# Performance work log

Hardware: AMD Instinct MI355X
Metric: run time of the kernel (lower is better)

The kernel has to match this reference:

```python
import jax, jax.numpy as jnp
import numpy as np

B, S, D, H, DF = 8, 1024, 1024, 16, 4096
DK = D // H
EPS = 1e-5


def setup_inputs() -> dict:
    key = jax.random.key(0)
    ks = jax.random.split(key, 16)
    w = lambda k, shape: (jax.random.normal(k, shape, jnp.float32) * 0.02)
    inp = {
        "x": jax.random.normal(ks[0], (B, S, D), jnp.float32),
        "mask": jnp.ones((B, 1, 1, S), jnp.int32),
        # attention projections (torch Linear: y = x @ W.T + b)
        "Wq": w(ks[1], (D, D)), "bq": jnp.zeros((D,), jnp.float32),
        "Wk": w(ks[2], (D, D)), "bk": jnp.zeros((D,), jnp.float32),
        "Wv": w(ks[3], (D, D)), "bv": jnp.zeros((D,), jnp.float32),
        "Wo": w(ks[4], (D, D)), "bo": jnp.zeros((D,), jnp.float32),
        "ln_attn_g": jnp.ones((D,), jnp.float32), "ln_attn_b": jnp.zeros((D,), jnp.float32),
        # feed-forward
        "W1": w(ks[5], (DF, D)), "b1": jnp.zeros((DF,), jnp.float32),
        "W2": w(ks[6], (D, DF)), "b2": jnp.zeros((D,), jnp.float32),
        "ln_ff_g": jnp.ones((D,), jnp.float32), "ln_ff_b": jnp.zeros((D,), jnp.float32),
        # BatchNorm1d(d_ff) inside FFN (eval mode: running stats)
        "bnff_g": jnp.ones((DF,), jnp.float32), "bnff_b": jnp.zeros((DF,), jnp.float32),
        "bnff_m": jnp.zeros((DF,), jnp.float32), "bnff_v": jnp.ones((DF,), jnp.float32),
        # BatchNorm1d(d_model) after each sublayer (eval mode)
        "bn1_g": jnp.ones((D,), jnp.float32), "bn1_b": jnp.zeros((D,), jnp.float32),
        "bn1_m": jnp.zeros((D,), jnp.float32), "bn1_v": jnp.ones((D,), jnp.float32),
        "bn2_g": jnp.ones((D,), jnp.float32), "bn2_b": jnp.zeros((D,), jnp.float32),
        "bn2_m": jnp.zeros((D,), jnp.float32), "bn2_v": jnp.ones((D,), jnp.float32),
    }
    return inp


def _layernorm(x, g, b):
    mu = jnp.mean(x, axis=-1, keepdims=True)
    var = jnp.mean(jnp.square(x - mu), axis=-1, keepdims=True)
    return (x - mu) * jax.lax.rsqrt(var + EPS) * g + b


def _batchnorm_eval(x, g, b, m, v):
    # x: [B,S,C]; BatchNorm1d over channel C (the transpose->bn->transpose in torch
    # is equivalent to per-channel affine normalization on the last dim in eval mode)
    return (x - m) * jax.lax.rsqrt(v + EPS) * g + b


def reference(x, mask, Wq, bq, Wk, bk, Wv, bv, Wo, bo, ln_attn_g, ln_attn_b,
              W1, b1, W2, b2, ln_ff_g, ln_ff_b,
              bnff_g, bnff_b, bnff_m, bnff_v,
              bn1_g, bn1_b, bn1_m, bn1_v,
              bn2_g, bn2_b, bn2_m, bn2_v):
    # ---- Multi-head self-attention (pre-LN on query/key/value input) ----
    xq = _layernorm(x, ln_attn_g, ln_attn_b)
    q = (xq @ Wq.T + bq).reshape(B, S, H, DK)
    k = (x @ Wk.T + bk).reshape(B, S, H, DK)   # note: original applies LN only to `query`;
    v = (x @ Wv.T + bv).reshape(B, S, H, DK)   # key/value are passed raw (same x here)
    scores = jnp.einsum("bqhd,bkhd->bhqk", q, k) / np.sqrt(DK).astype(np.float32)
    scores = jnp.where(mask == 0, jnp.float32(-1e9), scores)
    attn = jax.nn.softmax(scores, axis=-1)                      # [B,H,S,S]
    context = jnp.einsum("bhqk,bkhd->bqhd", attn, v).reshape(B, S, D)
    attn_out = context @ Wo.T + bo
    x = x + attn_out                                            # residual (eval: no dropout)
    x = _batchnorm_eval(x, bn1_g, bn1_b, bn1_m, bn1_v)
    # ---- Position-wise FFN ----
    xn = _layernorm(x, ln_ff_g, ln_ff_b)
    h = jax.nn.gelu(xn @ W1.T + b1, approximate=False)          # [B,S,DF]
    h = _batchnorm_eval(h, bnff_g, bnff_b, bnff_m, bnff_v)
    ff = h @ W2.T + b2
    x = x + ff
    x = _batchnorm_eval(x, bn2_g, bn2_b, bn2_m, bn2_v)
    return x, attn
```

## Files before the change

kernel.cpp:

```cpp
#include <hip/hip_runtime.h>
#include <hip/hip_bf16.h>
#include <math.h>

typedef __hip_bfloat16 bf16;
typedef __attribute__((ext_vector_type(8))) short short8;
typedef __attribute__((ext_vector_type(4))) short short4v;
typedef __attribute__((ext_vector_type(4))) float f32x4;

#define DEV static __device__ __forceinline__

DEV short f2bf(float f) {
    bf16 h = __float2bfloat16(f);
    return __builtin_bit_cast(short, h);
}

DEV void glds16(const void* g, void* l) {
    __builtin_amdgcn_global_load_lds((const __attribute__((address_space(1))) void*)g,
                                     (__attribute__((address_space(3))) void*)l, 16, 0, 0);
}

__global__ __launch_bounds__(256) void cast_all(const float* __restrict__ Wq,
                                                const float* __restrict__ Wk,
                                                const float* __restrict__ Wv,
                                                const float* __restrict__ Wo,
                                                const float* __restrict__ W1,
                                                const float* __restrict__ W2,
                                                bf16* __restrict__ wqkv, bf16* __restrict__ wo,
                                                bf16* __restrict__ w1, bf16* __restrict__ w2) {
    int i = blockIdx.x * 256 + threadIdx.x;
    const float* src;
    bf16* dst;
    int si, di;
    if (i < 786432) {
        src = (i < 262144) ? Wq : (i < 524288) ? Wk : Wv;
        si = (i < 262144) ? i : (i < 524288) ? i - 262144 : i - 524288;
        dst = wqkv; di = i;
    } else if (i < 1048576) {
        src = Wo; si = i - 786432; dst = wo; di = si;
    } else if (i < 2097152) {
        src = W1; si = i - 1048576; dst = w1; di = si;
    } else {
        src = W2; si = i - 2097152; dst = w2; di = si;
    }
    f32x4 v = ((const f32x4*)src)[si];
    short4v o;
    #pragma unroll
    for (int j = 0; j < 4; j++) o[j] = f2bf(v[j]);
    ((short4v*)dst)[di] = o;
}

__global__ __launch_bounds__(256) void affine_all(
    const float* __restrict__ g1, const float* __restrict__ bb1, const float* __restrict__ m1, const float* __restrict__ v1,
    const float* __restrict__ g2, const float* __restrict__ bb2, const float* __restrict__ m2, const float* __restrict__ v2,
    const float* __restrict__ gf, const float* __restrict__ bbf, const float* __restrict__ mf, const float* __restrict__ vf,
    float* __restrict__ s1, float* __restrict__ t1, float* __restrict__ s2, float* __restrict__ t2,
    float* __restrict__ sf, float* __restrict__ tf) {
    int i = blockIdx.x * 256 + threadIdx.x;
    const float *g, *b, *m, *v; float *s, *t; int j;
    if (i < 1024)      { g = g1; b = bb1; m = m1; v = v1; s = s1; t = t1; j = i; }
    else if (i < 2048) { g = g2; b = bb2; m = m2; v = v2; s = s2; t = t2; j = i - 1024; }
    else               { g = gf; b = bbf; m = mf; v = vf; s = sf; t = tf; j = i - 2048; }
    float sc = g[j] * rsqrtf(v[j] + 1e-5f);
    s[j] = sc;
    t[j] = b[j] - m[j] * sc;
}

__global__ __launch_bounds__(256) void ln_kernel(const float* __restrict__ x,
                                                 const float* __restrict__ g,
                                                 const float* __restrict__ b,
                                                 bf16* __restrict__ lnout,
                                                 bf16* __restrict__ rawout) {
    const int row = blockIdx.x, t = threadIdx.x;
    const float* xr = x + (size_t)row * 1024;
    f32x4 v = ((const f32x4*)xr)[t];
    float s = v[0] + v[1] + v[2] + v[3];
    float sq = v[0]*v[0] + v[1]*v[1] + v[2]*v[2] + v[3]*v[3];
    #pragma unroll
    for (int off = 1; off < 64; off <<= 1) {
        s  += __shfl_xor(s, off);
        sq += __shfl_xor(sq, off);
    }
    __shared__ float ls[4], lq[4];
    if ((t & 63) == 0) { ls[t >> 6] = s; lq[t >> 6] = sq; }
    __syncthreads();
    s = ls[0] + ls[1] + ls[2] + ls[3];
    sq = lq[0] + lq[1] + lq[2] + lq[3];
    float mu = s * (1.0f / 1024.0f);
    float rs = rsqrtf(sq * (1.0f / 1024.0f) - mu * mu + 1e-5f);
    f32x4 gg = ((const f32x4*)g)[t];
    f32x4 bb = ((const f32x4*)b)[t];
    short4v o;
    #pragma unroll
    for (int j = 0; j < 4; j++) o[j] = f2bf((v[j] - mu) * rs * gg[j] + bb[j]);
    ((short4v*)(lnout + (size_t)row * 1024))[t] = o;
    if (rawout) {
        short4v r;
        #pragma unroll
        for (int j = 0; j < 4; j++) r[j] = f2bf(v[j]);
        ((short4v*)(rawout + (size_t)row * 1024))[t] = r;
    }
}

enum { M_RESBN = 0, M_GELU = 1, M_QKV = 2 };

template <int BN, int MODE>
__global__ __launch_bounds__(512, 2) void gemm8(
    const bf16* __restrict__ A0, const bf16* __restrict__ A1, const bf16* __restrict__ Bw,
    const float* __restrict__ b0, const float* __restrict__ b1, const float* __restrict__ b2,
    void* __restrict__ o0, void* __restrict__ o1, void* __restrict__ o2,
    const float* __restrict__ res, const float* __restrict__ sa, const float* __restrict__ ta,
    int N, int K) {
    constexpr int NB = BN / 64;
    constexpr int SB = BN * 128;
    constexpr int CW = BN / 4;
    constexpr int NF = CW / 16;
    __shared__ char smem[65536 + 2 * SB];

    const int tid = threadIdx.x, lane = tid & 63, wid = tid >> 6;
    const int gx = gridDim.x;
    const int n_wg = gx * gridDim.y;
    int lin = blockIdx.y * gx + blockIdx.x;
    lin = (lin & 7) * (n_wg >> 3) + (lin >> 3);
    const int bn = (lin % gx) * BN, bm = (lin / gx) << 8;

    const int wr = wid >> 2, wc = wid & 3;
    const int arow = lane & 15, hi = lane >> 4;
    const int xr = arow & 7;
    const int ck0 = (hi ^ xr) << 3;
    const int ck1 = ((4 + hi) ^ xr) << 3;
    const int rowA = wr * 128 + arow;
    const int rowB = wc * CW + arow;

    const bf16* Asel;
    if constexpr (MODE == M_QKV) Asel = (bn < 1024) ? A0 : A1;
    else                         Asel = A0;

    const int rS = tid >> 3;
    const int cXor = ((tid & 7) ^ (rS & 7)) << 3;
    const bf16* gA = Asel + (size_t)(bm + rS) * K + cXor;
    const bf16* gB = Bw   + (size_t)(bn + rS) * K + cXor;

    f32x4 acc[8][NF] = {};

    auto stA = [&](int t, int i) {
        glds16(gA + (size_t)i * 64 * K + t * 64,
               smem + ((t & 1) << 15) + i * 8192 + (wid << 10));
    };
    auto stB = [&](int t, int i) {
        glds16(gB + (size_t)i * 64 * K + t * 64,
               smem + 65536 + (t & 1) * SB + i * 8192 + (wid << 10));
    };

    const int NT = K >> 6;
    #pragma unroll
    for (int i = 0; i < NB; i++) stB(0, i);
    stA(0, 0); stA(0, 2); stA(0, 1); stA(0, 3);

#define PHASE(Q)                                                                              \
    do {                                                                                      \
        const short8 a00 = *(const short8*)(Ap + (rowA + (2*(Q)) * 16) * 64 + ck0);           \
        const short8 a01 = *(const short8*)(Ap + (rowA + (2*(Q)) * 16) * 64 + ck1);           \
        const short8 a10 = *(const short8*)(Ap + (rowA + (2*(Q)+1) * 16) * 64 + ck0);         \
        const short8 a11 = *(const short8*)(Ap + (rowA + (2*(Q)+1) * 16) * 64 + ck1);         \
        __builtin_amdgcn_s_setprio(1);                                                        \
        _Pragma("unroll")                                                                     \
        for (int n = 0; n < NF; n++) {                                                        \
            acc[2*(Q)][n]   = __builtin_amdgcn_mfma_f32_16x16x32_bf16(a00, bva[n], acc[2*(Q)][n], 0, 0, 0);   \
            acc[2*(Q)][n]   = __builtin_amdgcn_mfma_f32_16x16x32_bf16(a01, bvb[n], acc[2*(Q)][n], 0, 0, 0);   \
            acc[2*(Q)+1][n] = __builtin_amdgcn_mfma_f32_16x16x32_bf16(a10, bva[n], acc[2*(Q)+1][n], 0, 0, 0); \
            acc[2*(Q)+1][n] = __builtin_amdgcn_mfma_f32_16x16x32_bf16(a11, bvb[n], acc[2*(Q)+1][n], 0, 0, 0); \
        }                                                                                     \
        __builtin_amdgcn_s_setprio(0);                                                        \
    } while (0)

    for (int t = 0; t < NT; ++t) {
        const int p = t & 1;
        const bf16* Ap = (const bf16*)(smem + (p << 15));
        const bf16* Bp = (const bf16*)(smem + 65536 + p * SB);
        asm volatile("s_waitcnt vmcnt(2)" ::: "memory");
        __builtin_amdgcn_s_barrier();
        if (t + 1 < NT) {
            stB(t + 1, 0);
            if constexpr (NB == 4) stB(t + 1, 1);
        }
        short8 bva[NF], bvb[NF];
        #pragma unroll
        for (int n = 0; n < NF; n++) {
            bva[n] = *(const short8*)(Bp + (rowB + n * 16) * 64 + ck0);
            bvb[n] = *(const short8*)(Bp + (rowB + n * 16) * 64 + ck1);
        }
        PHASE(0);
        __builtin_amdgcn_s_barrier();
        if (t + 1 < NT) {
            if constexpr (NB == 4) { stB(t + 1, 2); stB(t + 1, 3); }
            else                   { stB(t + 1, 1); }
        }
        PHASE(1);
        if (t == NT - 1) asm volatile("s_waitcnt vmcnt(0)" ::: "memory");
        else if constexpr (NB == 4) asm volatile("s_waitcnt vmcnt(4)" ::: "memory");
        else                        asm volatile("s_waitcnt vmcnt(2)" ::: "memory");
        __builtin_amdgcn_s_barrier();
        if (t + 1 < NT) { stA(t + 1, 0); stA(t + 1, 2); }
        PHASE(2);
        __builtin_amdgcn_s_barrier();
        if (t + 1 < NT) { stA(t + 1, 1); stA(t + 1, 3); }
        PHASE(3);
    }
#undef PHASE

    #pragma unroll
    for (int mf = 0; mf < 8; mf++) {
        #pragma unroll
        for (int nf = 0; nf < NF; nf++) {
            const int col = bn + wc * CW + nf * 16 + arow;
            #pragma unroll
            for (int j = 0; j < 4; j++) {
                const int row = bm + wr * 128 + mf * 16 + hi * 4 + j;
                if constexpr (MODE == M_RESBN) {
                    float v = acc[mf][nf][j] + b0[col];
                    size_t idx = (size_t)row * N + col;
                    ((float*)o0)[idx] = (res[idx] + v) * sa[col] + ta[col];
                } else if constexpr (MODE == M_GELU) {
                    float v = acc[mf][nf][j] + b0[col];
                    float ge = 0.5f * v * (1.0f + erff(v * 0.70710678118f));
                    ((bf16*)o0)[(size_t)row * N + col] = __float2bfloat16(ge * sa[col] + ta[col]);
                } else {
                    const int reg = col >> 10, c = col & 1023;
                    const float bb = (reg == 0) ? b0[c] : (reg == 1) ? b1[c] : b2[c];
                    float v = acc[mf][nf][j] + bb;
                    if (reg == 0)
                        ((bf16*)o0)[(size_t)row * 1024 + c] = __float2bfloat16(v * 0.125f);
                    else if (reg == 1)
                        ((bf16*)o1)[(size_t)row * 1024 + c] = __float2bfloat16(v);
                    else
                        ((bf16*)o2)[((size_t)(row >> 10) << 20) + ((size_t)c << 10) + (row & 1023)] =
                            __float2bfloat16(v);
                }
            }
        }
    }
}

__global__ __launch_bounds__(512, 4) void fattn_kernel(const bf16* __restrict__ q,
                                                       const bf16* __restrict__ k,
                                                       const bf16* __restrict__ vT,
                                                       const int* __restrict__ mask,
                                                       float* __restrict__ attn,
                                                       bf16* __restrict__ ctx) {
    const int bh = blockIdx.y, b = bh >> 4, h = bh & 15;
    const int q0 = blockIdx.x << 5;
    const int tid = threadIdx.x, lane = tid & 63, wid = tid >> 6;
    const int kb = wid << 7;
    const int arow = lane & 15, hi = lane >> 4, koff = hi << 3;
    const int rbase = hi << 2;

    __shared__ char smem[67584];
    bf16* Plds = (bf16*)smem;
    float* redm = (float*)(smem + 65536);
    float* reds = (float*)(smem + 66560);

    short8 qf[2], qf2[2];
    #pragma unroll
    for (int m = 0; m < 2; m++) {
        const bf16* qp = q + ((size_t)((b << 10) + q0 + (m << 4) + arow) << 10) + (h << 6);
        qf[m]  = *(const short8*)(qp + koff);
        qf2[m] = *(const short8*)(qp + 32 + koff);
    }

    f32x4 acc[2][8];
    #pragma unroll
    for (int m = 0; m < 2; m++)
        #pragma unroll
        for (int n = 0; n < 8; n++) acc[m][n] = (f32x4){0.f, 0.f, 0.f, 0.f};

    const bf16* kpBase = k + ((size_t)((b << 10) + kb + arow) << 10) + (h << 6);
    short8 kf  = *(const short8*)(kpBase + koff);
    short8 kf2 = *(const short8*)(kpBase + 32 + koff);
    #pragma unroll
    for (int n = 0; n < 8; n++) {
        short8 kfn, kf2n;
        if (n < 7) {
            const bf16* kp = kpBase + ((size_t)(n + 1) << 14);
            kfn  = *(const short8*)(kp + koff);
            kf2n = *(const short8*)(kp + 32 + koff);
        }
        acc[0][n] = __builtin_amdgcn_mfma_f32_16x16x32_bf16(qf[0],  kf,  acc[0][n], 0, 0, 0);
        acc[0][n] = __builtin_amdgcn_mfma_f32_16x16x32_bf16(qf2[0], kf2, acc[0][n], 0, 0, 0);
        acc[1][n] = __builtin_amdgcn_mfma_f32_16x16x32_bf16(qf[1],  kf,  acc[1][n], 0, 0, 0);
        acc[1][n] = __builtin_amdgcn_mfma_f32_16x16x32_bf16(qf2[1], kf2, acc[1][n], 0, 0, 0);
        kf = kfn; kf2 = kf2n;
    }

    float rmax[2][4];
    #pragma unroll
    for (int m = 0; m < 2; m++)
        #pragma unroll
        for (int j = 0; j < 4; j++) rmax[m][j] = -3.0e38f;

    #pragma unroll
    for (int n = 0; n < 8; n++) {
        const float madd = mask[(b << 10) + kb + (n << 4) + arow] ? 0.0f : -1e9f;
        #pragma unroll
        for (int m = 0; m < 2; m++)
            #pragma unroll
            for (int j = 0; j < 4; j++) {
                acc[m][n][j] += madd;
                rmax[m][j] = fmaxf(rmax[m][j], acc[m][n][j]);
            }
    }
    #pragma unroll
    for (int off = 1; off < 16; off <<= 1)
        #pragma unroll
        for (int m = 0; m < 2; m++)
            #pragma unroll
            for (int j = 0; j < 4; j++) rmax[m][j] = fmaxf(rmax[m][j], __shfl_xor(rmax[m][j], off));

    float rsum[2][4] = {};
    #pragma unroll
    for (int n = 0; n < 8; n++)
        #pragma unroll
        for (int m = 0; m < 2; m++)
            #pragma unroll
            for (int j = 0; j < 4; j++) {
                float p = __expf(acc[m][n][j] - rmax[m][j]);
                acc[m][n][j] = p;
                rsum[m][j] += p;
            }
    #pragma unroll
    for (int off = 1; off < 16; off <<= 1)
        #pragma unroll
        for (int m = 0; m < 2; m++)
            #pragma unroll
            for (int j = 0; j < 4; j++) rsum[m][j] += __shfl_xor(rsum[m][j], off);

    if (arow == 0) {
        #pragma unroll
        for (int m = 0; m < 2; m++)
            #pragma unroll
            for (int j = 0; j < 4; j++) {
                const int qr = (m << 4) + rbase + j;
                redm[(qr << 3) + wid] = rmax[m][j];
                reds[(qr << 3) + wid] = rsum[m][j];
            }
    }
    __syncthreads();

    float fscale[2][4];
    #pragma unroll
    for (int m = 0; m < 2; m++)
        #pragma unroll
        for (int j = 0; j < 4; j++) {
            const int qr = (m << 4) + rbase + j;
            const float* mm = redm + (qr << 3);
            const float* ss = reds + (qr << 3);
            f32x4 m0 = *(const f32x4*)mm, m1 = *(const f32x4*)(mm + 4);
            f32x4 s0 = *(const f32x4*)ss, s1 = *(const f32x4*)(ss + 4);
            float gm = fmaxf(fmaxf(fmaxf(m0[0], m0[1]), fmaxf(m0[2], m0[3])),
                             fmaxf(fmaxf(m1[0], m1[1]), fmaxf(m1[2], m1[3])));
            float S = s0[0] * __expf(m0[0] - gm) + s0[1] * __expf(m0[1] - gm) +
                      s0[2] * __expf(m0[2] - gm) + s0[3] * __expf(m0[3] - gm) +
                      s1[0] * __expf(m1[0] - gm) + s1[1] * __expf(m1[1] - gm) +
                      s1[2] * __expf(m1[2] - gm) + s1[3] * __expf(m1[3] - gm);
            fscale[m][j] = __expf(rmax[m][j] - gm) / S;
        }

    const size_t obase = (((size_t)bh << 10) + q0) << 10;
    #pragma unroll
    for (int m = 0; m < 2; m++)
        #pragma unroll
        for (int j = 0; j < 4; j++) {
            const int qr = (m << 4) + rbase + j;
            float* orow = attn + obase + ((size_t)qr << 10) + kb;
            char* prow = (char*)Plds + (qr << 11);
            const int rx = (qr & 7) << 4;
            const float iv = fscale[m][j];
            #pragma unroll
            for (int n = 0; n < 8; n++) {
                float p = acc[m][n][j] * iv;
                orow[(n << 4) + arow] = p;
                *(bf16*)(prow + ((((kb + (n << 4) + arow)) << 1) ^ rx)) = __float2bfloat16(p);
            }
        }

    asm volatile("s_waitcnt lgkmcnt(0)" ::: "memory");
    __builtin_amdgcn_s_barrier();
    __builtin_amdgcn_sched_barrier(0);

    const int qh = wid >> 2, dh = wid & 3;
    const char* pbase = (char*)Plds + (((qh << 4) + arow) << 11);
    const int prx = (arow & 7) << 4;
    const bf16* vrow = vT + ((size_t)((b << 10) + (h << 6) + (dh << 4) + arow) << 10);
    f32x4 acc2 = (f32x4){0.f, 0.f, 0.f, 0.f};
    #pragma unroll 8
    for (int kt = 0; kt < 32; kt++) {
        short8 af  = *(const short8*)(pbase + (((kt << 6) + (hi << 4)) ^ prx));
        short8 bf2 = *(const short8*)(vrow + (kt << 5) + koff);
        acc2 = __builtin_amdgcn_mfma_f32_16x16x32_bf16(af, bf2, acc2, 0, 0, 0);
    }

    #pragma unroll
    for (int j = 0; j < 4; j++) {
        const int row = q0 + (qh << 4) + rbase + j;
        ctx[((size_t)((b << 10) + row) << 10) + (h << 6) + (dh << 4) + arow] =
            __float2bfloat16(acc2[j]);
    }
}

extern "C" void kernel_launch(void* const* d_in, const int* in_sizes, int n_in,
                              void* d_out, int out_size, void* d_ws, size_t ws_size,
                              hipStream_t stream) {
    (void)in_sizes; (void)n_in; (void)out_size; (void)ws_size;
    const float* x   = (const float*)d_in[0];
    const int*   mask= (const int*)d_in[1];
    const float* Wq  = (const float*)d_in[2];  const float* bq  = (const float*)d_in[3];
    const float* Wk  = (const float*)d_in[4];  const float* bk  = (const float*)d_in[5];
    const float* Wv  = (const float*)d_in[6];  const float* bv  = (const float*)d_in[7];
    const float* Wo  = (const float*)d_in[8];  const float* bo  = (const float*)d_in[9];
    const float* lag = (const float*)d_in[10]; const float* lab = (const float*)d_in[11];
    const float* W1  = (const float*)d_in[12]; const float* b1  = (const float*)d_in[13];
    const float* W2  = (const float*)d_in[14]; const float* b2  = (const float*)d_in[15];
    const float* lfg = (const float*)d_in[16]; const float* lfb = (const float*)d_in[17];
    const float* bffg= (const float*)d_in[18]; const float* bffb= (const float*)d_in[19];
    const float* bffm= (const float*)d_in[20]; const float* bffv= (const float*)d_in[21];
    const float* b1g = (const float*)d_in[22]; const float* b1b = (const float*)d_in[23];
    const float* b1m = (const float*)d_in[24]; const float* b1v = (const float*)d_in[25];
    const float* b2g = (const float*)d_in[26]; const float* b2b = (const float*)d_in[27];
    const float* b2m = (const float*)d_in[28]; const float* b2v = (const float*)d_in[29];

    char* ws = (char*)d_ws;
    const size_t MB = 1024 * 1024;
    bf16* wqkv_bf = (bf16*)(ws);
    bf16* wo_bf   = (bf16*)(ws + 6 * MB);
    bf16* w1_bf   = (bf16*)(ws + 8 * MB);
    bf16* w2_bf   = (bf16*)(ws + 16 * MB);
    float* s1  = (float*)(ws + 24 * MB); float* t1  = s1 + 1024;
    float* s2  = t1 + 1024;              float* t2  = s2 + 1024;
    float* sff = t2 + 1024;              float* tff = sff + 4096;
    bf16* x_bf   = (bf16*)(ws + 25 * MB);
    bf16* xq_bf  = (bf16*)(ws + 41 * MB);
    bf16* q_bf   = (bf16*)(ws + 57 * MB);
    bf16* k_bf   = (bf16*)(ws + 73 * MB);
    bf16* vT_bf  = (bf16*)(ws + 89 * MB);
    bf16* ctx_bf = (bf16*)(ws + 105 * MB);
    float* x1    = (float*)(ws + 121 * MB);
    bf16* xn_bf  = (bf16*)(ws + 153 * MB);
    bf16* h_bf   = (bf16*)(ws + 169 * MB);

    float* out_x    = (float*)d_out;
    float* out_attn = out_x + (size_t)8 * 1024 * 1024;

    cast_all<<<12288, 256, 0, stream>>>(Wq, Wk, Wv, Wo, W1, W2, wqkv_bf, wo_bf, w1_bf, w2_bf);
    affine_all<<<24, 256, 0, stream>>>(b1g, b1b, b1m, b1v, b2g, b2b, b2m, b2v,
                                       bffg, bffb, bffm, bffv, s1, t1, s2, t2, sff, tff);

    ln_kernel<<<8192, 256, 0, stream>>>(x, lag, lab, xq_bf, x_bf);

    gemm8<128, M_QKV><<<dim3(24, 32), 512, 0, stream>>>(
        xq_bf, x_bf, wqkv_bf, bq, bk, bv, q_bf, k_bf, vT_bf, nullptr, nullptr, nullptr, 1024, 1024);

    fattn_kernel<<<dim3(32, 128), 512, 0, stream>>>(q_bf, k_bf, vT_bf, mask, out_attn, ctx_bf);

    gemm8<128, M_RESBN><<<dim3(8, 32), 512, 0, stream>>>(
        ctx_bf, nullptr, wo_bf, bo, nullptr, nullptr, x1, nullptr, nullptr, x, s1, t1, 1024, 1024);

    ln_kernel<<<8192, 256, 0, stream>>>(x1, lfg, lfb, xn_bf, nullptr);
    gemm8<256, M_GELU><<<dim3(16, 32), 512, 0, stream>>>(
        xn_bf, nullptr, w1_bf, b1, nullptr, nullptr, h_bf, nullptr, nullptr, nullptr, sff, tff, 4096, 1024);
    gemm8<128, M_RESBN><<<dim3(8, 32), 512, 0, stream>>>(
        h_bf, nullptr, w2_bf, b2, nullptr, nullptr, out_x, nullptr, nullptr, x1, s2, t2, 1024, 4096);
}
```

Before: 624.8 us.

## Add triple-buffered GEMM with interleaved async LDS loads for QKV, Wo, W2

Introduces a new GEMM kernel that uses a three-stage shared-memory ring (144KB LDS). It issues global-to-LDS loads two K-tiles ahead, interleaved between MFMA phases, with raised wave priority around the MFMAs and a remapped block order. The 256x128 tile is applied to the QKV projection, the output projection and the second FFN GEMM. The aim is to hide memory latency behind compute. In exchange, occupancy drops to a single workgroup per CU because of the large LDS footprint.

```diff
diff --git a/kernel.cpp b/kernel.cpp
--- a/kernel.cpp
+++ b/kernel.cpp
@@ -241,6 +241,126 @@
     }
 }
 
+template <int MODE>
+__global__ __launch_bounds__(512, 2) void gemm3s(
+    const bf16* __restrict__ A0, const bf16* __restrict__ A1, const bf16* __restrict__ Bw,
+    const float* __restrict__ b0, const float* __restrict__ b1, const float* __restrict__ b2,
+    void* __restrict__ o0, void* __restrict__ o1, void* __restrict__ o2,
+    const float* __restrict__ res, const float* __restrict__ sa, const float* __restrict__ ta,
+    int N, int K) {
+    __shared__ char smem[147456];
+
+    const int tid = threadIdx.x, lane = tid & 63, wid = tid >> 6;
+    const int gx = gridDim.x;
+    const int n_wg = gx * gridDim.y;
+    int lin = blockIdx.y * gx + blockIdx.x;
+    lin = (lin & 7) * (n_wg >> 3) + (lin >> 3);
+    const int bn = (lin % gx) << 7, bm = (lin / gx) << 8;
+
+    const int wr = wid >> 2, wc = wid & 3;
+    const int arow = lane & 15, hi = lane >> 4;
+    const int xr = arow & 7;
+    const int ck0 = (hi ^ xr) << 3;
+    const int ck1 = ((4 + hi) ^ xr) << 3;
+    const int rowA = wr * 128 + arow;
+    const int rowB = wc * 32 + arow;
+
+    const bf16* Asel;
+    if constexpr (MODE == M_QKV) Asel = (bn < 1024) ? A0 : A1;
+    else                         Asel = A0;
+
+    const int rS = tid >> 3;
+    const int cXor = ((tid & 7) ^ (rS & 7)) << 3;
+    const bf16* gA = Asel + (size_t)(bm + rS) * K + cXor;
+    const bf16* gB = Bw   + (size_t)(bn + rS) * K + cXor;
+
+    f32x4 acc[8][2] = {};
+
+    auto stA = [&](int t, int i) {
+        glds16(gA + (size_t)i * 64 * K + t * 64,
+               smem + (t % 3) * 32768 + i * 8192 + (wid << 10));
+    };
+    auto stB = [&](int t, int i) {
+        glds16(gB + (size_t)i * 64 * K + t * 64,
+               smem + 98304 + (t % 3) * 16384 + i * 8192 + (wid << 10));
+    };
+
+    const int NT = K >> 6;
+    stB(0, 0); stB(0, 1); stA(0, 0); stA(0, 2); stA(0, 1); stA(0, 3);
+    stB(1, 0); stB(1, 1); stA(1, 0); stA(1, 2); stA(1, 1); stA(1, 3);
+
+#define PHASE3(Q)                                                                             \
+    do {                                                                                      \
+        const short8 a00 = *(const short8*)(Ap + (rowA + (2*(Q)) * 16) * 64 + ck0);           \
+        const short8 a01 = *(const short8*)(Ap + (rowA + (2*(Q)) * 16) * 64 + ck1);           \
+        const short8 a10 = *(const short8*)(Ap + (rowA + (2*(Q)+1) * 16) * 64 + ck0);         \
+        const short8 a11 = *(const short8*)(Ap + (rowA + (2*(Q)+1) * 16) * 64 + ck1);         \
+        __builtin_amdgcn_s_setprio(1);                                                        \
+        _Pragma("unroll")                                                                     \
+        for (int n = 0; n < 2; n++) {                                                         \
+            acc[2*(Q)][n]   = __builtin_amdgcn_mfma_f32_16x16x32_bf16(a00, bva[n], acc[2*(Q)][n], 0, 0, 0);   \
+            acc[2*(Q)][n]   = __builtin_amdgcn_mfma_f32_16x16x32_bf16(a01, bvb[n], acc[2*(Q)][n], 0, 0, 0);   \
+            acc[2*(Q)+1][n] = __builtin_amdgcn_mfma_f32_16x16x32_bf16(a10, bva[n], acc[2*(Q)+1][n], 0, 0, 0); \
+            acc[2*(Q)+1][n] = __builtin_amdgcn_mfma_f32_16x16x32_bf16(a11, bvb[n], acc[2*(Q)+1][n], 0, 0, 0); \
+        }                                                                                     \
+        __builtin_amdgcn_s_setprio(0);                                                        \
+    } while (0)
+
+    for (int t = 0; t < NT; ++t) {
+        const bf16* Ap = (const bf16*)(smem + (t % 3) * 32768);
+        const bf16* Bp = (const bf16*)(smem + 98304 + (t % 3) * 16384);
+        if (t >= NT - 1) asm volatile("s_waitcnt vmcnt(0)" ::: "memory");
+        else             asm volatile("s_waitcnt vmcnt(6)" ::: "memory");
+        __builtin_amdgcn_s_barrier();
+        if (t + 2 < NT) { stB(t + 2, 0); stB(t + 2, 1); }
+        short8 bva[2], bvb[2];
+        #pragma unroll
+        for (int n = 0; n < 2; n++) {
+            bva[n] = *(const short8*)(Bp + (rowB + n * 16) * 64 + ck0);
+            bvb[n] = *(const short8*)(Bp + (rowB + n * 16) * 64 + ck1);
+        }
+        PHASE3(0);
+        PHASE3(1);
+        if (t + 2 < NT) { stA(t + 2, 0); stA(t + 2, 2); }
+        PHASE3(2);
+        if (t + 2 < NT) { stA(t + 2, 1); stA(t + 2, 3); }
+        PHASE3(3);
+    }
+#undef PHASE3
+
+    #pragma unroll
+    for (int mf = 0; mf < 8; mf++) {
+        #pragma unroll
+        for (int nf = 0; nf < 2; nf++) {
+            const int col = bn + wc * 32 + nf * 16 + arow;
+            #pragma unroll
+            for (int j = 0; j < 4; j++) {
+                const int row = bm + wr * 128 + mf * 16 + hi * 4 + j;
+                if constexpr (MODE == M_RESBN) {
+                    float v = acc[mf][nf][j] + b0[col];
+                    size_t idx = (size_t)row * N + col;
+                    ((float*)o0)[idx] = (res[idx] + v) * sa[col] + ta[col];
+                } else if constexpr (MODE == M_GELU) {
+                    float v = acc[mf][nf][j] + b0[col];
+                    float ge = 0.5f * v * (1.0f + erff(v * 0.70710678118f));
+                    ((bf16*)o0)[(size_t)row * N + col] = __float2bfloat16(ge * sa[col] + ta[col]);
+                } else {
+                    const int reg = col >> 10, c = col & 1023;
+                    const float bb = (reg == 0) ? b0[c] : (reg == 1) ? b1[c] : b2[c];
+                    float v = acc[mf][nf][j] + bb;
+                    if (reg == 0)
+                        ((bf16*)o0)[(size_t)row * 1024 + c] = __float2bfloat16(v * 0.125f);
+                    else if (reg == 1)
+                        ((bf16*)o1)[(size_t)row * 1024 + c] = __float2bfloat16(v);
+                    else
+                        ((bf16*)o2)[((size_t)(row >> 10) << 20) + ((size_t)c << 10) + (row & 1023)] =
+                            __float2bfloat16(v);
+                }
+            }
+        }
+    }
+}
+
 __global__ __launch_bounds__(512, 4) void fattn_kernel(const bf16* __restrict__ q,
                                                        const bf16* __restrict__ k,
                                                        const bf16* __restrict__ vT,
@@ -455,17 +575,17 @@
 
     ln_kernel<<<8192, 256, 0, stream>>>(x, lag, lab, xq_bf, x_bf);
 
-    gemm8<128, M_QKV><<<dim3(24, 32), 512, 0, stream>>>(
+    gemm3s<M_QKV><<<dim3(24, 32), 512, 0, stream>>>(
         xq_bf, x_bf, wqkv_bf, bq, bk, bv, q_bf, k_bf, vT_bf, nullptr, nullptr, nullptr, 1024, 1024);
 
     fattn_kernel<<<dim3(32, 128), 512, 0, stream>>>(q_bf, k_bf, vT_bf, mask, out_attn, ctx_bf);
 
-    gemm8<128, M_RESBN><<<dim3(8, 32), 512, 0, stream>>>(
+    gemm3s<M_RESBN><<<dim3(8, 32), 512, 0, stream>>>(
         ctx_bf, nullptr, wo_bf, bo, nullptr, nullptr, x1, nullptr, nullptr, x, s1, t1, 1024, 1024);
 
     ln_kernel<<<8192, 256, 0, stream>>>(x1, lfg, lfb, xn_bf, nullptr);
     gemm8<256, M_GELU><<<dim3(16, 32), 512, 0, stream>>>(
         xn_bf, nullptr, w1_bf, b1, nullptr, nullptr, h_bf, nullptr, nullptr, nullptr, sff, tff, 4096, 1024);
-    gemm8<128, M_RESBN><<<dim3(8, 32), 512, 0, stream>>>(
+    gemm3s<M_RESBN><<<dim3(8, 32), 512, 0, stream>>>(
         h_bf, nullptr, w2_bf, b2, nullptr, nullptr, out_x, nullptr, nullptr, x1, s2, t2, 1024, 4096);
 }
```

Result: faster. 606.5 us (-2.9%).

## Triple-buffer GEMM LDS pipeline with one barrier per k-step; nontemporal attn stores

Applied to the files above, without the earlier changes.

The GEMM now uses three LDS stages and prefetches tile t+2, replacing the double buffer that needed four barriers and split loads per k-step. This leaves a single barrier per iteration, to cut synchronisation stalls and hide global-load latency better. The tile width is fixed at 128 for every GEMM, so the FFN up-projection grid doubles to 32x32. The larger LDS footprint (144 KB) limits residency to one workgroup per CU. Separately, the fp32 attention-probability output is written with nontemporal stores to reduce cache pollution from that large streaming write.

```diff
diff --git a/kernel.cpp b/kernel.cpp
--- a/kernel.cpp
+++ b/kernel.cpp
@@ -103,25 +103,21 @@
 
 enum { M_RESBN = 0, M_GELU = 1, M_QKV = 2 };
 
-template <int BN, int MODE>
-__global__ __launch_bounds__(512, 2) void gemm8(
+template <int MODE>
+__global__ __launch_bounds__(512, 2) void gemm3s(
     const bf16* __restrict__ A0, const bf16* __restrict__ A1, const bf16* __restrict__ Bw,
     const float* __restrict__ b0, const float* __restrict__ b1, const float* __restrict__ b2,
     void* __restrict__ o0, void* __restrict__ o1, void* __restrict__ o2,
     const float* __restrict__ res, const float* __restrict__ sa, const float* __restrict__ ta,
     int N, int K) {
-    constexpr int NB = BN / 64;
-    constexpr int SB = BN * 128;
-    constexpr int CW = BN / 4;
-    constexpr int NF = CW / 16;
-    __shared__ char smem[65536 + 2 * SB];
+    __shared__ char smem[147456];
 
     const int tid = threadIdx.x, lane = tid & 63, wid = tid >> 6;
     const int gx = gridDim.x;
     const int n_wg = gx * gridDim.y;
     int lin = blockIdx.y * gx + blockIdx.x;
     lin = (lin & 7) * (n_wg >> 3) + (lin >> 3);
-    const int bn = (lin % gx) * BN, bm = (lin / gx) << 8;
+    const int bn = (lin % gx) << 7, bm = (lin / gx) << 8;
 
     const int wr = wid >> 2, wc = wid & 3;
     const int arow = lane & 15, hi = lane >> 4;
@@ -129,7 +125,7 @@
     const int ck0 = (hi ^ xr) << 3;
     const int ck1 = ((4 + hi) ^ xr) << 3;
     const int rowA = wr * 128 + arow;
-    const int rowB = wc * CW + arow;
+    const int rowB = wc * 32 + arow;
 
     const bf16* Asel;
     if constexpr (MODE == M_QKV) Asel = (bn < 1024) ? A0 : A1;
@@ -140,23 +136,22 @@
     const bf16* gA = Asel + (size_t)(bm + rS) * K + cXor;
     const bf16* gB = Bw   + (size_t)(bn + rS) * K + cXor;
 
-    f32x4 acc[8][NF] = {};
+    f32x4 acc[8][2] = {};
 
     auto stA = [&](int t, int i) {
         glds16(gA + (size_t)i * 64 * K + t * 64,
-               smem + ((t & 1) << 15) + i * 8192 + (wid << 10));
+               smem + (t % 3) * 32768 + i * 8192 + (wid << 10));
     };
     auto stB = [&](int t, int i) {
         glds16(gB + (size_t)i * 64 * K + t * 64,
-               smem + 65536 + (t & 1) * SB + i * 8192 + (wid << 10));
+               smem + 98304 + (t % 3) * 16384 + i * 8192 + (wid << 10));
     };
 
     const int NT = K >> 6;
-    #pragma unroll
-    for (int i = 0; i < NB; i++) stB(0, i);
-    stA(0, 0); stA(0, 2); stA(0, 1); stA(0, 3);
-
-#define PHASE(Q)                                                                              \
+    stB(0, 0); stB(0, 1); stA(0, 0); stA(0, 2); stA(0, 1); stA(0, 3);
+    stB(1, 0); stB(1, 1); stA(1, 0); stA(1, 2); stA(1, 1); stA(1, 3);
+
+#define PHASE3(Q)                                                                             \
     do {                                                                                      \
         const short8 a00 = *(const short8*)(Ap + (rowA + (2*(Q)) * 16) * 64 + ck0);           \
         const short8 a01 = *(const short8*)(Ap + (rowA + (2*(Q)) * 16) * 64 + ck1);           \
@@ -164,7 +159,7 @@
         const short8 a11 = *(const short8*)(Ap + (rowA + (2*(Q)+1) * 16) * 64 + ck1);         \
         __builtin_amdgcn_s_setprio(1);                                                        \
         _Pragma("unroll")                                                                     \
-        for (int n = 0; n < NF; n++) {                                                        \
+        for (int n = 0; n < 2; n++) {                                                         \
             acc[2*(Q)][n]   = __builtin_amdgcn_mfma_f32_16x16x32_bf16(a00, bva[n], acc[2*(Q)][n], 0, 0, 0);   \
             acc[2*(Q)][n]   = __builtin_amdgcn_mfma_f32_16x16x32_bf16(a01, bvb[n], acc[2*(Q)][n], 0, 0, 0);   \
             acc[2*(Q)+1][n] = __builtin_amdgcn_mfma_f32_16x16x32_bf16(a10, bva[n], acc[2*(Q)+1][n], 0, 0, 0); \
@@ -174,45 +169,32 @@
     } while (0)
 
     for (int t = 0; t < NT; ++t) {
-        const int p = t & 1;
-        const bf16* Ap = (const bf16*)(smem + (p << 15));
-        const bf16* Bp = (const bf16*)(smem + 65536 + p * SB);
-        asm volatile("s_waitcnt vmcnt(2)" ::: "memory");
+        const bf16* Ap = (const bf16*)(smem + (t % 3) * 32768);
+        const bf16* Bp = (const bf16*)(smem + 98304 + (t % 3) * 16384);
+        if (t >= NT - 1) asm volatile("s_waitcnt vmcnt(0)" ::: "memory");
+        else             asm volatile("s_waitcnt vmcnt(6)" ::: "memory");
         __builtin_amdgcn_s_barrier();
-        if (t + 1 < NT) {
-            stB(t + 1, 0);
-            if constexpr (NB == 4) stB(t + 1, 1);
-        }
-        short8 bva[NF], bvb[NF];
-        #pragma unroll
-        for (int n = 0; n < NF; n++) {
+        if (t + 2 < NT) { stB(t + 2, 0); stB(t + 2, 1); }
+        short8 bva[2], bvb[2];
+        #pragma unroll
+        for (int n = 0; n < 2; n++) {
             bva[n] = *(const short8*)(Bp + (rowB + n * 16) * 64 + ck0);
             bvb[n] = *(const short8*)(Bp + (rowB + n * 16) * 64 + ck1);
         }
-        PHASE(0);
-        __builtin_amdgcn_s_barrier();
-        if (t + 1 < NT) {
-            if constexpr (NB == 4) { stB(t + 1, 2); stB(t + 1, 3); }
-            else                   { stB(t + 1, 1); }
-        }
-        PHASE(1);
-        if (t == NT - 1) asm volatile("s_waitcnt vmcnt(0)" ::: "memory");
-        else if constexpr (NB == 4) asm volatile("s_waitcnt vmcnt(4)" ::: "memory");
-        else                        asm volatile("s_waitcnt vmcnt(2)" ::: "memory");
-        __builtin_amdgcn_s_barrier();
-        if (t + 1 < NT) { stA(t + 1, 0); stA(t + 1, 2); }
-        PHASE(2);
-        __builtin_amdgcn_s_barrier();
-        if (t + 1 < NT) { stA(t + 1, 1); stA(t + 1, 3); }
-        PHASE(3);
-    }
-#undef PHASE
+        PHASE3(0);
+        PHASE3(1);
+        if (t + 2 < NT) { stA(t + 2, 0); stA(t + 2, 2); }
+        PHASE3(2);
+        if (t + 2 < NT) { stA(t + 2, 1); stA(t + 2, 3); }
+        PHASE3(3);
+    }
+#undef PHASE3
 
     #pragma unroll
     for (int mf = 0; mf < 8; mf++) {
         #pragma unroll
-        for (int nf = 0; nf < NF; nf++) {
-            const int col = bn + wc * CW + nf * 16 + arow;
+        for (int nf = 0; nf < 2; nf++) {
+            const int col = bn + wc * 32 + nf * 16 + arow;
             #pragma unroll
             for (int j = 0; j < 4; j++) {
                 const int row = bm + wr * 128 + mf * 16 + hi * 4 + j;
@@ -377,7 +359,7 @@
             #pragma unroll
             for (int n = 0; n < 8; n++) {
                 float p = acc[m][n][j] * iv;
-                orow[(n << 4) + arow] = p;
+                __builtin_nontemporal_store(p, orow + (n << 4) + arow);
                 *(bf16*)(prow + ((((kb + (n << 4) + arow)) << 1) ^ rx)) = __float2bfloat16(p);
             }
         }
@@ -455,17 +437,17 @@
 
     ln_kernel<<<8192, 256, 0, stream>>>(x, lag, lab, xq_bf, x_bf);
 
-    gemm8<128, M_QKV><<<dim3(24, 32), 512, 0, stream>>>(
+    gemm3s<M_QKV><<<dim3(24, 32), 512, 0, stream>>>(
         xq_bf, x_bf, wqkv_bf, bq, bk, bv, q_bf, k_bf, vT_bf, nullptr, nullptr, nullptr, 1024, 1024);
 
     fattn_kernel<<<dim3(32, 128), 512, 0, stream>>>(q_bf, k_bf, vT_bf, mask, out_attn, ctx_bf);
 
-    gemm8<128, M_RESBN><<<dim3(8, 32), 512, 0, stream>>>(
+    gemm3s<M_RESBN><<<dim3(8, 32), 512, 0, stream>>>(
         ctx_bf, nullptr, wo_bf, bo, nullptr, nullptr, x1, nullptr, nullptr, x, s1, t1, 1024, 1024);
 
     ln_kernel<<<8192, 256, 0, stream>>>(x1, lfg, lfb, xn_bf, nullptr);
-    gemm8<256, M_GELU><<<dim3(16, 32), 512, 0, stream>>>(
+    gemm3s<M_GELU><<<dim3(32, 32), 512, 0, stream>>>(
         xn_bf, nullptr, w1_bf, b1, nullptr, nullptr, h_bf, nullptr, nullptr, nullptr, sff, tff, 4096, 1024);
-    gemm8<128, M_RESBN><<<dim3(8, 32), 512, 0, stream>>>(
+    gemm3s<M_RESBN><<<dim3(8, 32), 512, 0, stream>>>(
         h_bf, nullptr, w2_bf, b2, nullptr, nullptr, out_x, nullptr, nullptr, x1, s2, t2, 1024, 4096);
 }
```

Measured after the change: 591.4 us (median of 2 runs). -5.3%, faster.
